# Optimization experiments

Hardware: AMD Instinct MI355X
Metric: run time of the kernel (lower is better)

The kernel has to match this reference:

```python
import jax, jax.numpy as jnp
import numpy as np

N, L, S, H, D = 1, 4096, 4096, 8, 32


def setup_inputs() -> dict:
    key = jax.random.key(0)
    k1, k2, k3 = jax.random.split(key, 3)
    q = jax.random.normal(k1, (N, L, H, D), dtype=jnp.float32)
    k = jax.random.normal(k2, (N, S, H, D), dtype=jnp.float32)
    v = jax.random.normal(k3, (N, S, H, D), dtype=jnp.float32)
    q_mask = jnp.ones((N, L), dtype=bool)
    kv_mask = jnp.ones((N, S), dtype=bool)
    return {"q": q, "k": k, "v": v, "q_mask": q_mask, "kv_mask": kv_mask}


def reference(q, k, v, q_mask, kv_mask):
    # qk: [N, L, S, H] -- full score tensor as in the torch module
    qk = jnp.einsum('nlhd,nshd->nlsh', q, k)
    # mask BEFORE scaling (matches torch: masked_fill then divide by sqrt(D))
    mask = ~(q_mask[:, :, None, None] & kv_mask[:, None, :, None])
    qk = jnp.where(mask, jnp.float32(-1e9), qk)
    scale = q.shape[3] ** 0.5
    attn = jax.nn.softmax(qk / scale, axis=2)  # softmax over S
    out = jnp.einsum('nlsh,nshd->nlhd', attn, v)
    return out
```

## Files before the change

### kernel.cpp

```cpp
#include <hip/hip_runtime.h>
#include <hip/hip_bf16.h>

typedef __bf16 bf16x4 __attribute__((ext_vector_type(4)));
typedef __bf16 bf16x8 __attribute__((ext_vector_type(8)));
typedef float  f32x4  __attribute__((ext_vector_type(4)));

#define H_  8
#define D_  32
#define L_  4096
#define S_  4096
#define BM  64
#define BN  64
#define NSPLIT 4

static __device__ __forceinline__ f32x4 mfma_k16(bf16x4 a, bf16x4 b, f32x4 c) {
#if __has_builtin(__builtin_amdgcn_mfma_f32_16x16x16_bf16)
    return __builtin_amdgcn_mfma_f32_16x16x16_bf16(a, b, c, 0, 0, 0);
#elif __has_builtin(__builtin_amdgcn_mfma_f32_16x16x16bf16_1k)
    typedef short s16x4 __attribute__((ext_vector_type(4)));
    union U { bf16x4 h; s16x4 s; };
    U ua, ub; ua.h = a; ub.h = b;
    return __builtin_amdgcn_mfma_f32_16x16x16bf16_1k(ua.s, ub.s, c, 0, 0, 0);
#else
    asm("v_mfma_f32_16x16x16_bf16 %0, %1, %2, %0" : "+v"(c) : "v"(a), "v"(b));
    return c;
#endif
}

template<bool DIRECT>
__global__ __launch_bounds__(256, 6)
void fattn_main(const float* __restrict__ q, const float* __restrict__ kk,
                const float* __restrict__ v, float* __restrict__ num,
                float* __restrict__ den, float* __restrict__ out, int schunk)
{
    const int qt = blockIdx.x, h = blockIdx.y, sp = blockIdx.z;
    const int tid = threadIdx.x, wave = tid >> 6, lane = tid & 63;
    const int col = lane & 15, quad = lane >> 4;

    __shared__ __align__(16) __bf16 Ks[2][BN][40];
    __shared__ __align__(16) __bf16 Vt[2][D_][72];

    const float cs = 0.17677669529663687f * 1.4426950408889634f;

    const int qn = qt * BM + wave * 16 + col;
    bf16x8 qb;
    {
        const float* qp = q + ((size_t)qn * H_ + h) * D_ + quad * 8;
        float4 q0 = *(const float4*)qp;
        float4 q1 = *(const float4*)(qp + 4);
        qb[0]=(__bf16)(q0.x*cs); qb[1]=(__bf16)(q0.y*cs);
        qb[2]=(__bf16)(q0.z*cs); qb[3]=(__bf16)(q0.w*cs);
        qb[4]=(__bf16)(q1.x*cs); qb[5]=(__bf16)(q1.y*cs);
        qb[6]=(__bf16)(q1.z*cs); qb[7]=(__bf16)(q1.w*cs);
    }

    f32x4 o0 = {0,0,0,0}, o1 = {0,0,0,0}, accl = {0,0,0,0};
    const f32x4 zc = {0,0,0,0};
    const bf16x4 ones = {(__bf16)1.f, (__bf16)1.f, (__bf16)1.f, (__bf16)1.f};

    const int srow = tid >> 2;
    const int g    = tid & 3;
    const int dseg = g * 8;
    const int vcol = (srow + 16 * g) & 63;
    const int rot0 = (col >> 3) << 4;

    const int sbeg = sp * schunk;
    const int T = schunk / BN;

    float4 kf0, kf1, vf0, vf1;
    {
        const size_t goff = ((size_t)(sbeg + srow) * H_ + h) * D_ + dseg;
        kf0 = *(const float4*)(kk + goff);
        kf1 = *(const float4*)(kk + goff + 4);
        vf0 = *(const float4*)(v + goff);
        vf1 = *(const float4*)(v + goff + 4);
    }
    float4 kn0 = kf0, kn1 = kf1, vn0 = vf0, vn1 = vf1;

    for (int t = 0; t < T; ++t) {
        const int b = t & 1;
        {
            bf16x8 kb;
            kb[0]=(__bf16)kf0.x; kb[1]=(__bf16)kf0.y; kb[2]=(__bf16)kf0.z; kb[3]=(__bf16)kf0.w;
            kb[4]=(__bf16)kf1.x; kb[5]=(__bf16)kf1.y; kb[6]=(__bf16)kf1.z; kb[7]=(__bf16)kf1.w;
            *(bf16x8*)(&Ks[b][srow][dseg]) = kb;
            float vv[8] = {vf0.x, vf0.y, vf0.z, vf0.w, vf1.x, vf1.y, vf1.z, vf1.w};
#pragma unroll
            for (int j = 0; j < 8; ++j)
                Vt[b][dseg + j][vcol] = (__bf16)vv[j];
        }
        if (t + 1 < T) {
            const size_t goff = ((size_t)(sbeg + (t+1)*BN + srow) * H_ + h) * D_ + dseg;
            kn0 = *(const float4*)(kk + goff);
            kn1 = *(const float4*)(kk + goff + 4);
            vn0 = *(const float4*)(v + goff);
            vn1 = *(const float4*)(v + goff + 4);
        }
        __syncthreads();

#pragma unroll
        for (int sb = 0; sb < 4; ++sb) {
            bf16x8 ka = *(const bf16x8*)(&Ks[b][sb * 16 + col][quad * 8]);
            f32x4 st = __builtin_amdgcn_mfma_f32_16x16x32_bf16(ka, qb, zc, 0, 0, 0);
            bf16x4 pb;
#pragma unroll
            for (int r = 0; r < 4; ++r)
                pb[r] = (__bf16)__builtin_amdgcn_exp2f(st[r]);
            const int sc  = sb * 16 + quad * 4;
            bf16x4 va0 = *(const bf16x4*)(&Vt[b][col     ][(sc + rot0)      & 63]);
            bf16x4 va1 = *(const bf16x4*)(&Vt[b][col + 16][(sc + rot0 + 32) & 63]);
            o0   = mfma_k16(va0,  pb, o0);
            o1   = mfma_k16(va1,  pb, o1);
            accl = mfma_k16(ones, pb, accl);
        }
        kf0 = kn0; kf1 = kn1; vf0 = vn0; vf1 = vn1;
    }

    if (DIRECT) {
        const float inv = 1.f / accl[0];
        float* op = out + ((size_t)qn * H_ + h) * D_;
        f32x4 r0 = {o0[0]*inv, o0[1]*inv, o0[2]*inv, o0[3]*inv};
        f32x4 r1 = {o1[0]*inv, o1[1]*inv, o1[2]*inv, o1[3]*inv};
        *(f32x4*)(op + quad * 4)      = r0;
        *(f32x4*)(op + 16 + quad * 4) = r1;
    } else {
        float* pr = num + (((size_t)(sp * H_ + h) * L_ + qn) << 5);
        *(f32x4*)(pr + quad * 4)      = o0;
        *(f32x4*)(pr + 16 + quad * 4) = o1;
        if (quad == 0) den[(size_t)(sp * H_ + h) * L_ + qn] = accl[0];
    }
}

__global__ __launch_bounds__(256)
void fattn_combine(const float* __restrict__ num, const float* __restrict__ den,
                   float* __restrict__ out)
{
    const int i  = blockIdx.x * 256 + threadIdx.x;
    const int d4 = (i & 7) * 4;
    const int h  = (i >> 3) & 7;
    const int l  = i >> 6;
    f32x4 acc = {0,0,0,0};
    float dn = 0.f;
    for (int sp = 0; sp < NSPLIT; ++sp) {
        const float* pr = num + (((size_t)(sp * H_ + h) * L_ + l) << 5) + d4;
        f32x4 t = *(const f32x4*)pr;
        acc[0] += t[0]; acc[1] += t[1]; acc[2] += t[2]; acc[3] += t[3];
        dn += den[(size_t)(sp * H_ + h) * L_ + l];
    }
    const float inv = 1.f / dn;
    f32x4 r = {acc[0]*inv, acc[1]*inv, acc[2]*inv, acc[3]*inv};
    *(f32x4*)(out + ((size_t)l * H_ + h) * D_ + d4) = r;
}

extern "C" void kernel_launch(void* const* d_in, const int* in_sizes, int n_in,
                              void* d_out, int out_size, void* d_ws, size_t ws_size,
                              hipStream_t stream) {
    const float* q = (const float*)d_in[0];
    const float* k = (const float*)d_in[1];
    const float* v = (const float*)d_in[2];
    float* out = (float*)d_out;
    const size_t nnum = (size_t)NSPLIT * H_ * L_ * 32;
    const size_t nden = (size_t)NSPLIT * H_ * L_;
    if (ws_size >= (nnum + nden) * sizeof(float)) {
        float* num = (float*)d_ws;
        float* den = num + nnum;
        fattn_main<false><<<dim3(L_ / BM, H_, NSPLIT), 256, 0, stream>>>(
            q, k, v, num, den, out, S_ / NSPLIT);
        fattn_combine<<<dim3((L_ * H_ * D_ / 4) / 256), 256, 0, stream>>>(num, den, out);
    } else {
        fattn_main<true><<<dim3(L_ / BM, H_, 1), 256, 0, stream>>>(
            q, k, v, nullptr, nullptr, out, S_);
    }
}
```

Before: 112.5 us.

## Pre-convert K and V to bf16 head-major layouts before attention

Adds two prep kernels: one converts K to bf16 in a [H,S,D] layout, the other converts V to bf16 and transposes it to [H,D,S]. The main attention kernel then loads contiguous bf16 tiles and writes them straight to shared memory. This removes the repeated fp32 loads and per-block conversion and transposition that each of the 64 query tiles did for K/V. In exchange it adds two extra launches, a global round trip of the bf16 copies, and a larger workspace requirement.

```diff
diff --git a/kernel.cpp b/kernel.cpp
--- a/kernel.cpp
+++ b/kernel.cpp
@@ -27,6 +27,118 @@
 #endif
 }
 
+__global__ __launch_bounds__(256)
+void prep_k(const float* __restrict__ kk, __bf16* __restrict__ kb)
+{
+    const int oi = blockIdx.x * 256 + threadIdx.x;
+    const int h    = oi >> 14;
+    const int s    = (oi >> 2) & (S_ - 1);
+    const int dseg = (oi & 3) * 8;
+    const float* ip = kk + (((size_t)s * H_ + h) * D_ + dseg);
+    float4 a = *(const float4*)ip, b = *(const float4*)(ip + 4);
+    bf16x8 o;
+    o[0]=(__bf16)a.x; o[1]=(__bf16)a.y; o[2]=(__bf16)a.z; o[3]=(__bf16)a.w;
+    o[4]=(__bf16)b.x; o[5]=(__bf16)b.y; o[6]=(__bf16)b.z; o[7]=(__bf16)b.w;
+    *(bf16x8*)(kb + ((size_t)h * S_ + s) * D_ + dseg) = o;
+}
+
+__global__ __launch_bounds__(256)
+void prep_v(const float* __restrict__ v, __bf16* __restrict__ vt)
+{
+    const int h  = blockIdx.y;
+    const int s0 = blockIdx.x * 64;
+    __shared__ __bf16 T[D_][72];
+    const int sr = threadIdx.x >> 2, dseg = (threadIdx.x & 3) * 8;
+    const float* ip = v + (((size_t)(s0 + sr) * H_ + h) * D_ + dseg);
+    float4 a = *(const float4*)ip, b = *(const float4*)(ip + 4);
+    float vv[8] = {a.x, a.y, a.z, a.w, b.x, b.y, b.z, b.w};
+#pragma unroll
+    for (int j = 0; j < 8; ++j) T[dseg + j][sr] = (__bf16)vv[j];
+    __syncthreads();
+    const int d = threadIdx.x >> 3, so = (threadIdx.x & 7) * 8;
+    bf16x8 o = *(const bf16x8*)(&T[d][so]);
+    *(bf16x8*)(vt + ((size_t)h * D_ + d) * S_ + s0 + so) = o;
+}
+
+__global__ __launch_bounds__(256, 6)
+void fattn_v2(const __bf16* __restrict__ kb, const __bf16* __restrict__ vtg,
+              const float* __restrict__ q, float* __restrict__ num,
+              float* __restrict__ den, int schunk)
+{
+    const int qt = blockIdx.x, h = blockIdx.y, sp = blockIdx.z;
+    const int tid = threadIdx.x, wave = tid >> 6, lane = tid & 63;
+    const int col = lane & 15, quad = lane >> 4;
+
+    __shared__ __align__(16) __bf16 Ks[2][BN][40];
+    __shared__ __align__(16) __bf16 Vt[2][D_][72];
+
+    const float cs = 0.17677669529663687f * 1.4426950408889634f;
+
+    const int qn = qt * BM + wave * 16 + col;
+    bf16x8 qb;
+    {
+        const float* qp = q + ((size_t)qn * H_ + h) * D_ + quad * 8;
+        float4 q0 = *(const float4*)qp;
+        float4 q1 = *(const float4*)(qp + 4);
+        qb[0]=(__bf16)(q0.x*cs); qb[1]=(__bf16)(q0.y*cs);
+        qb[2]=(__bf16)(q0.z*cs); qb[3]=(__bf16)(q0.w*cs);
+        qb[4]=(__bf16)(q1.x*cs); qb[5]=(__bf16)(q1.y*cs);
+        qb[6]=(__bf16)(q1.z*cs); qb[7]=(__bf16)(q1.w*cs);
+    }
+
+    f32x4 o0 = {0,0,0,0}, o1 = {0,0,0,0}, accl = {0,0,0,0};
+    const f32x4 zc = {0,0,0,0};
+    const bf16x4 ones = {(__bf16)1.f, (__bf16)1.f, (__bf16)1.f, (__bf16)1.f};
+
+    const int srow = tid >> 2, kseg = (tid & 3) * 8;
+    const int vd   = tid >> 3, vso  = (tid & 7) * 8;
+    const int vcolw = (vso + 16 * (vd >> 3)) & 63;
+    const int rot0  = (col >> 3) << 4;
+
+    const int sbeg = sp * schunk;
+    const int T = schunk / BN;
+
+    const __bf16* kptr = kb  + ((size_t)h * S_ + sbeg + srow) * D_ + kseg;
+    const __bf16* vptr = vtg + ((size_t)h * D_ + vd) * S_ + sbeg + vso;
+
+    bf16x8 kf = *(const bf16x8*)kptr;
+    bf16x8 vf = *(const bf16x8*)vptr;
+    bf16x8 kn = kf, vn = vf;
+
+    for (int t = 0; t < T; ++t) {
+        const int b = t & 1;
+        *(bf16x8*)(&Ks[b][srow][kseg]) = kf;
+        *(bf16x8*)(&Vt[b][vd][vcolw])  = vf;
+        if (t + 1 < T) {
+            kn = *(const bf16x8*)(kptr + (size_t)(t + 1) * BN * D_);
+            vn = *(const bf16x8*)(vptr + (t + 1) * BN);
+        }
+        __syncthreads();
+
+#pragma unroll
+        for (int sb = 0; sb < 4; ++sb) {
+            bf16x8 ka = *(const bf16x8*)(&Ks[b][sb * 16 + col][quad * 8]);
+            f32x4 st = __builtin_amdgcn_mfma_f32_16x16x32_bf16(ka, qb, zc, 0, 0, 0);
+            bf16x4 pb;
+#pragma unroll
+            for (int r = 0; r < 4; ++r)
+                pb[r] = (__bf16)__builtin_amdgcn_exp2f(st[r]);
+            const int sc  = sb * 16 + quad * 4;
+            bf16x4 va0 = *(const bf16x4*)(&Vt[b][col     ][(sc + rot0)      & 63]);
+            bf16x4 va1 = *(const bf16x4*)(&Vt[b][col + 16][(sc + rot0 + 32) & 63]);
+            o0   = mfma_k16(va0,  pb, o0);
+            o1   = mfma_k16(va1,  pb, o1);
+            accl = mfma_k16(ones, pb, accl);
+        }
+        kf = kn; vf = vn;
+    }
+
+    float* pr = num + (((size_t)(sp * H_ + h) * L_ + qn) << 5);
+    *(f32x4*)(pr + quad * 4)      = o0;
+    *(f32x4*)(pr + 16 + quad * 4) = o1;
+    if (quad == 0) den[(size_t)(sp * H_ + h) * L_ + qn] = accl[0];
+}
+
 template<bool DIRECT>
 __global__ __launch_bounds__(256, 6)
 void fattn_main(const float* __restrict__ q, const float* __restrict__ kk,
@@ -161,7 +273,19 @@
     float* out = (float*)d_out;
     const size_t nnum = (size_t)NSPLIT * H_ * L_ * 32;
     const size_t nden = (size_t)NSPLIT * H_ * L_;
-    if (ws_size >= (nnum + nden) * sizeof(float)) {
+    const size_t nkv  = (size_t)H_ * S_ * D_;
+    const size_t need_v2 = (nnum + nden) * sizeof(float) + 2 * nkv * sizeof(__bf16);
+    if (ws_size >= need_v2) {
+        float* num = (float*)d_ws;
+        float* den = num + nnum;
+        __bf16* kbp = (__bf16*)(den + nden);
+        __bf16* vtp = kbp + nkv;
+        prep_k<<<dim3((H_ * S_ * D_ / 8) / 256), 256, 0, stream>>>(k, kbp);
+        prep_v<<<dim3(S_ / 64, H_), 256, 0, stream>>>(v, vtp);
+        fattn_v2<<<dim3(L_ / BM, H_, NSPLIT), 256, 0, stream>>>(
+            kbp, vtp, q, num, den, S_ / NSPLIT);
+        fattn_combine<<<dim3((L_ * H_ * D_ / 4) / 256), 256, 0, stream>>>(num, den, out);
+    } else if (ws_size >= (nnum + nden) * sizeof(float)) {
         float* num = (float*)d_ws;
         float* den = num + nnum;
         fattn_main<false><<<dim3(L_ / BM, H_, NSPLIT), 256, 0, stream>>>(
```

After: 112.2 us. Within noise of the previous version (-0.3%).

## Use 32x32 MFMA tiles with 128-query blocks and permlane P relayout

Applied to the files above, without the earlier changes.

Adds a new split-S attention kernel in which each wave handles 32 queries using 32x32x16 bf16 MFMAs for both QK^T and PV. The probabilities are packed with v_cvt_pk_bf16_f32 and rearranged across half-waves with v_permlane32_swap, so they feed the PV MFMA directly from registers. The row sum is accumulated with VALU adds instead of an extra MFMA against ones. Each block now covers 128 queries, halving the number of K/V tile loads and conversions per query. The cost is fewer blocks (256 instead of 512) and higher register pressure, with launch bounds lowered to 4.

```diff
diff --git a/kernel.cpp b/kernel.cpp
--- a/kernel.cpp
+++ b/kernel.cpp
@@ -4,27 +4,141 @@
 typedef __bf16 bf16x4 __attribute__((ext_vector_type(4)));
 typedef __bf16 bf16x8 __attribute__((ext_vector_type(8)));
 typedef float  f32x4  __attribute__((ext_vector_type(4)));
+typedef float  f32x16 __attribute__((ext_vector_type(16)));
 
 #define H_  8
 #define D_  32
 #define L_  4096
 #define S_  4096
 #define BM  64
+#define BM4 128
 #define BN  64
 #define NSPLIT 4
 
 static __device__ __forceinline__ f32x4 mfma_k16(bf16x4 a, bf16x4 b, f32x4 c) {
 #if __has_builtin(__builtin_amdgcn_mfma_f32_16x16x16_bf16)
     return __builtin_amdgcn_mfma_f32_16x16x16_bf16(a, b, c, 0, 0, 0);
-#elif __has_builtin(__builtin_amdgcn_mfma_f32_16x16x16bf16_1k)
-    typedef short s16x4 __attribute__((ext_vector_type(4)));
-    union U { bf16x4 h; s16x4 s; };
-    U ua, ub; ua.h = a; ub.h = b;
-    return __builtin_amdgcn_mfma_f32_16x16x16bf16_1k(ua.s, ub.s, c, 0, 0, 0);
 #else
     asm("v_mfma_f32_16x16x16_bf16 %0, %1, %2, %0" : "+v"(c) : "v"(a), "v"(b));
     return c;
 #endif
+}
+
+__global__ __launch_bounds__(256, 4)
+void fattn_v6(const float* __restrict__ q, const float* __restrict__ kk,
+              const float* __restrict__ v, float* __restrict__ num,
+              float* __restrict__ den, int schunk)
+{
+    const int qt = blockIdx.x, h = blockIdx.y, sp = blockIdx.z;
+    const int tid = threadIdx.x, wq = tid >> 6, lane = tid & 63;
+    const int ln = lane & 31, hl = lane >> 5;
+
+    __shared__ __align__(16) __bf16 Ks[2][64][40];
+    __shared__ __align__(16) __bf16 Vt[2][D_][72];
+
+    const float cs = 0.17677669529663687f * 1.4426950408889634f;
+
+    const int qn = qt * BM4 + wq * 32 + ln;
+    bf16x8 qf0, qf1;
+    {
+        const float* qp = q + ((size_t)qn * H_ + h) * D_ + hl * 8;
+        float4 a = *(const float4*)qp,        b2 = *(const float4*)(qp + 4);
+        float4 c = *(const float4*)(qp + 16), d2 = *(const float4*)(qp + 20);
+        qf0[0]=(__bf16)(a.x*cs);  qf0[1]=(__bf16)(a.y*cs);
+        qf0[2]=(__bf16)(a.z*cs);  qf0[3]=(__bf16)(a.w*cs);
+        qf0[4]=(__bf16)(b2.x*cs); qf0[5]=(__bf16)(b2.y*cs);
+        qf0[6]=(__bf16)(b2.z*cs); qf0[7]=(__bf16)(b2.w*cs);
+        qf1[0]=(__bf16)(c.x*cs);  qf1[1]=(__bf16)(c.y*cs);
+        qf1[2]=(__bf16)(c.z*cs);  qf1[3]=(__bf16)(c.w*cs);
+        qf1[4]=(__bf16)(d2.x*cs); qf1[5]=(__bf16)(d2.y*cs);
+        qf1[6]=(__bf16)(d2.z*cs); qf1[7]=(__bf16)(d2.w*cs);
+    }
+
+    f32x16 o = {0,0,0,0,0,0,0,0,0,0,0,0,0,0,0,0};
+    const f32x16 z16 = {0,0,0,0,0,0,0,0,0,0,0,0,0,0,0,0};
+    f32x4 accl = {0,0,0,0};
+
+    const int srow = tid >> 2, g = tid & 3, dseg = g * 8;
+    const int vcol = (srow + 16 * g) & 63;
+
+    const int sbeg = sp * schunk;
+    const int T = schunk / BN;
+
+    float4 kf0, kf1, vf0, vf1;
+    {
+        const size_t goff = ((size_t)(sbeg + srow) * H_ + h) * D_ + dseg;
+        kf0 = *(const float4*)(kk + goff);
+        kf1 = *(const float4*)(kk + goff + 4);
+        vf0 = *(const float4*)(v + goff);
+        vf1 = *(const float4*)(v + goff + 4);
+    }
+    float4 kn0 = kf0, kn1 = kf1, vn0 = vf0, vn1 = vf1;
+
+    for (int t = 0; t < T; ++t) {
+        const int b = t & 1;
+        {
+            bf16x8 kb8;
+            kb8[0]=(__bf16)kf0.x; kb8[1]=(__bf16)kf0.y; kb8[2]=(__bf16)kf0.z; kb8[3]=(__bf16)kf0.w;
+            kb8[4]=(__bf16)kf1.x; kb8[5]=(__bf16)kf1.y; kb8[6]=(__bf16)kf1.z; kb8[7]=(__bf16)kf1.w;
+            *(bf16x8*)(&Ks[b][srow][dseg]) = kb8;
+            float vv[8] = {vf0.x, vf0.y, vf0.z, vf0.w, vf1.x, vf1.y, vf1.z, vf1.w};
+#pragma unroll
+            for (int j = 0; j < 8; ++j)
+                Vt[b][dseg + j][vcol] = (__bf16)vv[j];
+        }
+        if (t + 1 < T) {
+            const size_t goff = ((size_t)(sbeg + (t+1)*BN + srow) * H_ + h) * D_ + dseg;
+            kn0 = *(const float4*)(kk + goff);
+            kn1 = *(const float4*)(kk + goff + 4);
+            vn0 = *(const float4*)(v + goff);
+            vn1 = *(const float4*)(v + goff + 4);
+        }
+        __syncthreads();
+
+#pragma unroll
+        for (int sh = 0; sh < 2; ++sh) {
+            bf16x8 ka0 = *(const bf16x8*)(&Ks[b][sh * 32 + ln][hl * 8]);
+            bf16x8 ka1 = *(const bf16x8*)(&Ks[b][sh * 32 + ln][16 + hl * 8]);
+            f32x16 st = __builtin_amdgcn_mfma_f32_32x32x16_bf16(ka0, qf0, z16, 0, 0, 0);
+            st = __builtin_amdgcn_mfma_f32_32x32x16_bf16(ka1, qf1, st, 0, 0, 0);
+#pragma unroll
+            for (int u = 0; u < 2; ++u) {
+                float p[8];
+#pragma unroll
+                for (int r = 0; r < 8; ++r) p[r] = __builtin_amdgcn_exp2f(st[u*8 + r]);
+                accl[u*2]     += p[0] + p[1] + p[2] + p[3];
+                accl[u*2 + 1] += p[4] + p[5] + p[6] + p[7];
+                unsigned A, B, C, D;
+                asm("v_cvt_pk_bf16_f32 %0, %1, %2" : "=v"(A) : "v"(p[0]), "v"(p[1]));
+                asm("v_cvt_pk_bf16_f32 %0, %1, %2" : "=v"(B) : "v"(p[2]), "v"(p[3]));
+                asm("v_cvt_pk_bf16_f32 %0, %1, %2" : "=v"(C) : "v"(p[4]), "v"(p[5]));
+                asm("v_cvt_pk_bf16_f32 %0, %1, %2" : "=v"(D) : "v"(p[6]), "v"(p[7]));
+                asm("v_permlane32_swap_b32 %0, %1" : "+v"(A), "+v"(C));
+                asm("v_permlane32_swap_b32 %0, %1" : "+v"(B), "+v"(D));
+                union { unsigned w[4]; bf16x8 f; } pb;
+                pb.w[0] = A; pb.w[1] = B; pb.w[2] = C; pb.w[3] = D;
+                const int slot = sh * 2 + u;
+                const int vb = (slot * 16 + 8 * hl + 16 * (ln >> 3)) & 63;
+                bf16x8 va = *(const bf16x8*)(&Vt[b][ln][vb]);
+                o = __builtin_amdgcn_mfma_f32_32x32x16_bf16(va, pb.f, o, 0, 0, 0);
+            }
+        }
+        kf0 = kn0; kf1 = kn1; vf0 = vn0; vf1 = vn1;
+    }
+
+    float dsum = accl[0] + accl[1] + accl[2] + accl[3];
+    dsum += __shfl_xor(dsum, 32, 64);
+
+    float* pr = num + (((size_t)(sp * H_ + h) * L_ + qn) << 5);
+    f32x4 w0 = {o[0],  o[1],  o[2],  o[3]};
+    f32x4 w1 = {o[4],  o[5],  o[6],  o[7]};
+    f32x4 w2 = {o[8],  o[9],  o[10], o[11]};
+    f32x4 w3 = {o[12], o[13], o[14], o[15]};
+    *(f32x4*)(pr      + hl * 4) = w0;
+    *(f32x4*)(pr + 8  + hl * 4) = w1;
+    *(f32x4*)(pr + 16 + hl * 4) = w2;
+    *(f32x4*)(pr + 24 + hl * 4) = w3;
+    if (hl == 0) den[(size_t)(sp * H_ + h) * L_ + qn] = dsum;
 }
 
 template<bool DIRECT>
@@ -164,8 +278,8 @@
     if (ws_size >= (nnum + nden) * sizeof(float)) {
         float* num = (float*)d_ws;
         float* den = num + nnum;
-        fattn_main<false><<<dim3(L_ / BM, H_, NSPLIT), 256, 0, stream>>>(
-            q, k, v, num, den, out, S_ / NSPLIT);
+        fattn_v6<<<dim3(L_ / BM4, H_, NSPLIT), 256, 0, stream>>>(
+            q, k, v, num, den, S_ / NSPLIT);
         fattn_combine<<<dim3((L_ * H_ * D_ / 4) / 256), 256, 0, stream>>>(num, den, out);
     } else {
         fattn_main<true><<<dim3(L_ / BM, H_, 1), 256, 0, stream>>>(
```

Measured after the change: 104.8 us. 1.07x faster.
